# Kernel optimization log

Measured on AMD Instinct MI355X. Metric: run time of the kernel, lower is better.

## Reference

```python
import jax, jax.numpy as jnp
import numpy as np

N = 50000    # nodes
E = 800000   # edges (avg degree 16)
IN = 256     # in_dim
HID = 256    # hidden_dim
OUT = 128    # out_dim


def setup_inputs() -> dict:
    key = jax.random.key(0)
    ks = jax.random.split(key, 9)
    features = jax.random.normal(ks[0], (N, IN), jnp.float32)
    src = jax.random.randint(ks[1], (E,), 0, N, jnp.int32)
    dst = jax.random.randint(ks[2], (E,), 0, N, jnp.int32)
    noise = jax.random.normal(ks[3], (N, OUT), jnp.float32)
    def glorot(k, shape, fan):
        return jax.random.normal(k, shape, jnp.float32) / np.float32(np.sqrt(fan))
    W1 = glorot(ks[4], (IN, HID), IN);  b1 = jnp.zeros((HID,), jnp.float32)
    W2 = glorot(ks[5], (HID, OUT), HID); b2 = jnp.zeros((OUT,), jnp.float32)
    W3 = glorot(ks[6], (HID, OUT), HID); b3 = jnp.zeros((OUT,), jnp.float32)
    fcW = glorot(ks[7], (HID, IN), IN)   # nn.Linear(in_dim, hidden_dim).weight: [HID, IN]
    return dict(features=features, noise=noise, W1=W1, b1=b1, W2=W2, b2=b2,
                W3=W3, b3=b3, fcW=fcW, src=src, dst=dst)


def _gcn(x, W, b, src, dst, out_norm, in_norm):
    """DGL GraphConv norm='both': D_out^{-1/2} A D_in^{-1/2} X W + b."""
    x = x * out_norm[:, None]          # scale src features by out-deg^{-1/2}
    x = x @ W                          # dense transform (order commutes with SpMM)
    agg = jax.ops.segment_sum(x[src], dst, num_segments=N)  # sparse aggregate
    return agg * in_norm[:, None] + b


def reference(features, noise, W1, b1, W2, b2, W3, b3, fcW, src, dst):
    ones = jnp.ones((E,), jnp.float32)
    out_deg = jax.ops.segment_sum(ones, src, num_segments=N)
    in_deg = jax.ops.segment_sum(ones, dst, num_segments=N)
    out_norm = jnp.maximum(out_deg, 1.0) ** -0.5
    in_norm = jnp.maximum(in_deg, 1.0) ** -0.5

    h = jax.nn.relu(_gcn(features, W1, b1, src, dst, out_norm, in_norm))
    mean = jax.nn.relu(_gcn(h, W2, b2, src, dst, out_norm, in_norm))
    log_std = _gcn(h, W3, b3, src, dst, out_norm, in_norm)  # identity activation
    z = mean + noise * jnp.exp(log_std)
    seq_fts = features @ fcW.T
    return z, h, seq_fts
```

## Files before the change

kernel.cpp:

```cpp
#include <hip/hip_runtime.h>
#include <hip/hip_bf16.h>
#include <stdint.h>

#define IN_DIM 256
#define HID_DIM 256
#define OUT_DIM 128

typedef __attribute__((ext_vector_type(8))) short short8;
typedef __attribute__((ext_vector_type(4))) float floatx4;

__device__ __forceinline__ float bf2f(ushort u) {
  union { uint32_t i; float f; } v; v.i = ((uint32_t)u) << 16; return v.f;
}
__device__ __forceinline__ ushort f2bf(float f) {
  union { float f; uint32_t u; } v; v.f = f;
  uint32_t u = v.u;
  uint32_t r = u + 0x7fffu + ((u >> 16) & 1u);
  return (ushort)(r >> 16);
}

__global__ void f2b_kernel(const float* __restrict__ in, ushort* __restrict__ out, int n) {
  int base = (blockIdx.x * 256 + threadIdx.x) * 4;
  if (base < n) {
    float4 v = *(const float4*)(in + base);
    ushort4 o;
    o.x = f2bf(v.x); o.y = f2bf(v.y); o.z = f2bf(v.z); o.w = f2bf(v.w);
    *(ushort4*)(out + base) = o;
  }
}

__global__ void deg_kernel(const int* __restrict__ src, const int* __restrict__ dst,
                           int* __restrict__ out_deg, int* __restrict__ in_deg, int E) {
  int e = blockIdx.x * 256 + threadIdx.x;
  if (e < E) {
    atomicAdd(&out_deg[src[e]], 1);
    atomicAdd(&in_deg[dst[e]], 1);
  }
}

__global__ void norm_kernel(const int* __restrict__ out_deg, const int* __restrict__ in_deg,
                            float* __restrict__ out_norm, float* __restrict__ in_norm, int N) {
  int n = blockIdx.x * 256 + threadIdx.x;
  if (n < N) {
    int od = out_deg[n]; if (od < 1) od = 1;
    int id = in_deg[n];  if (id < 1) id = 1;
    out_norm[n] = rsqrtf((float)od);
    in_norm[n]  = rsqrtf((float)id);
  }
}

__global__ void scan_sums(const int* __restrict__ deg, int* __restrict__ chunk_sum, int n) {
  __shared__ int lds[256];
  int b = blockIdx.x, t = threadIdx.x;
  int base = b * 1024 + t * 4;
  int s = 0;
  if (base + 3 < n) {
    int4 v = *(const int4*)(deg + base);
    s = v.x + v.y + v.z + v.w;
  } else {
    for (int i = 0; i < 4; ++i) if (base + i < n) s += deg[base + i];
  }
  lds[t] = s;
  __syncthreads();
  for (int off = 128; off > 0; off >>= 1) {
    if (t < off) lds[t] += lds[t + off];
    __syncthreads();
  }
  if (t == 0) chunk_sum[b] = lds[0];
}

__global__ void scan_chunks(const int* __restrict__ chunk_sum, int* __restrict__ chunk_off,
                            int nchunks, int* __restrict__ row_ptr) {
  __shared__ int lds[256];
  int t = threadIdx.x;
  int v = (t < nchunks) ? chunk_sum[t] : 0;
  lds[t] = v;
  __syncthreads();
  for (int off = 1; off < 256; off <<= 1) {
    int add = (t >= off) ? lds[t - off] : 0;
    __syncthreads();
    lds[t] += add;
    __syncthreads();
  }
  if (t < nchunks) chunk_off[t] = lds[t] - v;
  if (t == 0) row_ptr[0] = 0;
}

__global__ void scan_final(const int* __restrict__ deg, const int* __restrict__ chunk_off,
                           int* __restrict__ row_ptr, int n) {
  __shared__ int lds[256];
  int b = blockIdx.x, t = threadIdx.x;
  int base = b * 1024 + t * 4;
  int v[4]; int s = 0;
#pragma unroll
  for (int i = 0; i < 4; ++i) { v[i] = (base + i < n) ? deg[base + i] : 0; s += v[i]; }
  lds[t] = s;
  __syncthreads();
  for (int off = 1; off < 256; off <<= 1) {
    int add = (t >= off) ? lds[t - off] : 0;
    __syncthreads();
    lds[t] += add;
    __syncthreads();
  }
  int run = lds[t] - s + chunk_off[b];
#pragma unroll
  for (int i = 0; i < 4; ++i) {
    run += v[i];
    if (base + i < n) row_ptr[base + i + 1] = run;
  }
}

__global__ void fill_kernel(const int* __restrict__ src, const int* __restrict__ dst,
                            const int* __restrict__ row_ptr, int* __restrict__ fill_cnt,
                            const float* __restrict__ out_norm,
                            int* __restrict__ edge_src, float* __restrict__ edge_w, int E) {
  int e = blockIdx.x * 256 + threadIdx.x;
  if (e < E) {
    int d = dst[e];
    int s = src[e];
    int pos = row_ptr[d] + atomicAdd(&fill_cnt[d], 1);
    edge_src[pos] = s;
    edge_w[pos] = out_norm[s];
  }
}

__global__ void prep_weights(const float* __restrict__ W1, const float* __restrict__ W2,
                             const float* __restrict__ W3, const float* __restrict__ b2,
                             const float* __restrict__ b3, const float* __restrict__ fcW,
                             ushort* __restrict__ W1T, ushort* __restrict__ WcT,
                             float* __restrict__ bcat, ushort* __restrict__ fcWb) {
  int k = blockIdx.x;
  int n = threadIdx.x;
  W1T[n * 256 + k] = f2bf(W1[k * 256 + n]);
  WcT[n * 256 + k] = f2bf((n < 128) ? W2[k * 128 + n] : W3[k * 128 + (n - 128)]);
  fcWb[k * 256 + n] = f2bf(fcW[k * 256 + n]);
  if (k == 0) bcat[n] = (n < 128) ? b2[n] : b3[n - 128];
}

__global__ __launch_bounds__(256) void agg_kernel(
    const ushort* __restrict__ x, const int* __restrict__ row_ptr,
    const int* __restrict__ edge_src, const float* __restrict__ edge_w,
    const float* __restrict__ in_norm, ushort* __restrict__ out, int N) {
  int wave = threadIdx.x >> 6, lane = threadIdx.x & 63;
  int n = blockIdx.x * 4 + wave;
  if (n >= N) return;
  int half = lane >> 5;
  int hl = lane & 31;
  int start = row_ptr[n], end = row_ptr[n + 1];
  float acc[8];
#pragma unroll
  for (int k = 0; k < 8; ++k) acc[k] = 0.f;

  for (int base = start; base < end; base += 4) {
    int i0 = base + half;
    int i1 = base + 2 + half;
    int s0 = 0, s1 = 0; float w0 = 0.f, w1 = 0.f;
    if (i0 < end) { s0 = edge_src[i0]; w0 = edge_w[i0]; }
    if (i1 < end) { s1 = edge_src[i1]; w1 = edge_w[i1]; }
    uint4 v0 = *(const uint4*)&x[(size_t)s0 * 256 + hl * 8];
    uint4 v1 = *(const uint4*)&x[(size_t)s1 * 256 + hl * 8];
    const uint32_t* p0 = (const uint32_t*)&v0;
    const uint32_t* p1 = (const uint32_t*)&v1;
#pragma unroll
    for (int k = 0; k < 4; ++k) {
      acc[2 * k]     += bf2f((ushort)(p0[k] & 0xffffu)) * w0;
      acc[2 * k + 1] += bf2f((ushort)(p0[k] >> 16)) * w0;
      acc[2 * k]     += bf2f((ushort)(p1[k] & 0xffffu)) * w1;
      acc[2 * k + 1] += bf2f((ushort)(p1[k] >> 16)) * w1;
    }
  }
#pragma unroll
  for (int k = 0; k < 8; ++k) acc[k] += __shfl_xor(acc[k], 32, 64);

  if (half == 0) {
    float inn = in_norm[n];
    uint4 o;
    uint32_t* po = (uint32_t*)&o;
#pragma unroll
    for (int k = 0; k < 4; ++k) {
      po[k] = ((uint32_t)f2bf(acc[2 * k + 1] * inn) << 16) |
              (uint32_t)f2bf(acc[2 * k] * inn);
    }
    *(uint4*)&out[(size_t)n * 256 + hl * 8] = o;
  }
}

__global__ __launch_bounds__(256) void gemm_kernel(
    const ushort* __restrict__ A, const ushort* __restrict__ BT,
    const float* __restrict__ bias, float* __restrict__ C32,
    ushort* __restrict__ Cbf, int M, int Nout, int relu) {
  __shared__ alignas(16) ushort A_lds[128 * 72];
  __shared__ alignas(16) ushort B_lds[128 * 72];
  int t = threadIdx.x;
  int m0 = blockIdx.x * 128;
  int n0 = blockIdx.y * 128;
  int wave = t >> 6, lane = t & 63;
  int wm = (wave >> 1) * 64, wn = (wave & 1) * 64;
  int l15 = lane & 15, quad = lane >> 4;

  floatx4 acc[4][4];
#pragma unroll
  for (int i = 0; i < 4; ++i)
#pragma unroll
    for (int j = 0; j < 4; ++j) acc[i][j] = (floatx4)(0.f);

  for (int kc = 0; kc < 256; kc += 64) {
#pragma unroll
    for (int r = 0; r < 4; ++r) {
      int idx = t + r * 256;
      int row = idx >> 3;
      int c8 = (idx & 7) << 3;
      int grow = m0 + row; if (grow > M - 1) grow = M - 1;
      uint4 va = *(const uint4*)(A + (size_t)grow * 256 + kc + c8);
      *(uint4*)&A_lds[row * 72 + c8] = va;
      uint4 vb = *(const uint4*)(BT + (size_t)(n0 + row) * 256 + kc + c8);
      *(uint4*)&B_lds[row * 72 + c8] = vb;
    }
    __syncthreads();
#pragma unroll
    for (int ko = 0; ko < 2; ++ko) {
      short8 a[4], b[4];
#pragma unroll
      for (int i = 0; i < 4; ++i) {
        a[i] = *(const short8*)&A_lds[(wm + i * 16 + l15) * 72 + ko * 32 + quad * 8];
        b[i] = *(const short8*)&B_lds[(wn + i * 16 + l15) * 72 + ko * 32 + quad * 8];
      }
#pragma unroll
      for (int i = 0; i < 4; ++i)
#pragma unroll
        for (int j = 0; j < 4; ++j)
          acc[i][j] = __builtin_amdgcn_mfma_f32_16x16x32_bf16(a[i], b[j], acc[i][j], 0, 0, 0);
    }
    __syncthreads();
  }

#pragma unroll
  for (int i = 0; i < 4; ++i) {
#pragma unroll
    for (int j = 0; j < 4; ++j) {
      int col = n0 + wn + j * 16 + l15;
      float bv = bias ? bias[col] : 0.f;
#pragma unroll
      for (int r = 0; r < 4; ++r) {
        int row = m0 + wm + i * 16 + quad * 4 + r;
        if (row < M) {
          float v = acc[i][j][r] + bv;
          if (relu) v = fmaxf(v, 0.f);
          size_t o = (size_t)row * Nout + col;
          if (C32) C32[o] = v;
          if (Cbf) Cbf[o] = f2bf(v);
        }
      }
    }
  }
}

__global__ void z_kernel(const ushort* __restrict__ tmp, const float* __restrict__ noise,
                         float* __restrict__ z, int N) {
  int idx = blockIdx.x * 256 + threadIdx.x;
  if (idx < N * OUT_DIM) {
    int n = idx >> 7, c = idx & 127;
    float m = bf2f(tmp[(size_t)n * 256 + c]);
    float ls = bf2f(tmp[(size_t)n * 256 + 128 + c]);
    float zz = fmaxf(m, 0.f) + noise[idx] * expf(ls);
    z[idx] = zz;
  }
}

extern "C" void kernel_launch(void* const* d_in, const int* in_sizes, int n_in,
                              void* d_out, int out_size, void* d_ws, size_t ws_size,
                              hipStream_t stream) {
  const float* features = (const float*)d_in[0];
  const float* noise    = (const float*)d_in[1];
  const float* W1 = (const float*)d_in[2];
  const float* b1 = (const float*)d_in[3];
  const float* W2 = (const float*)d_in[4];
  const float* b2 = (const float*)d_in[5];
  const float* W3 = (const float*)d_in[6];
  const float* b3 = (const float*)d_in[7];
  const float* fcW = (const float*)d_in[8];
  const int* src = (const int*)d_in[9];
  const int* dst = (const int*)d_in[10];
  const int N = in_sizes[0] / IN_DIM;
  const int E = in_sizes[9];

  float* out = (float*)d_out;
  float* z_out = out;
  float* h_out = out + (size_t)N * OUT_DIM;
  float* s_out = h_out + (size_t)N * HID_DIM;

  char* w = (char*)d_ws;
  auto carve = [&](size_t bytes) {
    char* p = w;
    w += (bytes + 255) & ~(size_t)255;
    return p;
  };
  ushort* feat_bf = (ushort*)carve((size_t)N * 256 * 2);
  ushort* h_bf    = (ushort*)carve((size_t)N * 256 * 2);
  ushort* agg_buf = (ushort*)carve((size_t)N * 256 * 2);
  ushort* tmp_bf  = (ushort*)carve((size_t)N * 256 * 2);
  ushort* W1T  = (ushort*)carve(256 * 256 * 2);
  ushort* WcT  = (ushort*)carve(256 * 256 * 2);
  ushort* fcWb = (ushort*)carve(256 * 256 * 2);
  float*  bcat = (float*)carve(256 * 4);
  int* degs    = (int*)carve((size_t)3 * N * 4);
  int* out_deg = degs;
  int* in_deg  = degs + N;
  int* fill_cnt = degs + 2 * N;
  float* out_norm = (float*)carve((size_t)N * 4);
  float* in_norm  = (float*)carve((size_t)N * 4);
  int* row_ptr  = (int*)carve((size_t)(N + 1) * 4);
  int* edge_src = (int*)carve((size_t)E * 4);
  float* edge_w = (float*)carve((size_t)E * 4);
  int* chunk_sum = (int*)carve(256 * 4);
  int* chunk_off = (int*)carve(256 * 4);

  const int nchunks = (N + 1023) / 1024;

  hipMemsetAsync(degs, 0, (size_t)3 * N * 4, stream);
  deg_kernel<<<(E + 255) / 256, 256, 0, stream>>>(src, dst, out_deg, in_deg, E);
  norm_kernel<<<(N + 255) / 256, 256, 0, stream>>>(out_deg, in_deg, out_norm, in_norm, N);
  scan_sums<<<nchunks, 256, 0, stream>>>(in_deg, chunk_sum, N);
  scan_chunks<<<1, 256, 0, stream>>>(chunk_sum, chunk_off, nchunks, row_ptr);
  scan_final<<<nchunks, 256, 0, stream>>>(in_deg, chunk_off, row_ptr, N);
  fill_kernel<<<(E + 255) / 256, 256, 0, stream>>>(src, dst, row_ptr, fill_cnt, out_norm,
                                                   edge_src, edge_w, E);

  f2b_kernel<<<((N * 256 / 4) + 255) / 256, 256, 0, stream>>>(features, feat_bf, N * 256);
  prep_weights<<<256, 256, 0, stream>>>(W1, W2, W3, b2, b3, fcW, W1T, WcT, bcat, fcWb);

  dim3 ggrid((N + 127) / 128, 2);
  agg_kernel<<<(N + 3) / 4, 256, 0, stream>>>(feat_bf, row_ptr, edge_src, edge_w, in_norm, agg_buf, N);
  gemm_kernel<<<ggrid, 256, 0, stream>>>(agg_buf, W1T, b1, h_out, h_bf, N, 256, 1);
  agg_kernel<<<(N + 3) / 4, 256, 0, stream>>>(h_bf, row_ptr, edge_src, edge_w, in_norm, agg_buf, N);
  gemm_kernel<<<ggrid, 256, 0, stream>>>(agg_buf, WcT, bcat, (float*)nullptr, tmp_bf, N, 256, 0);
  z_kernel<<<(N * OUT_DIM + 255) / 256, 256, 0, stream>>>(tmp_bf, noise, z_out, N);
  gemm_kernel<<<ggrid, 256, 0, stream>>>(feat_bf, fcWb, (const float*)nullptr, s_out, (ushort*)nullptr, N, 256, 0);
}
```

Measured before the change: 587.9 us.

## Fuse z computation into GEMM epilogue, widen GEMM tile, drop norm kernel

The GEMM now computes a full 128x256 output tile per block, so mean and log_std columns sit in the same block, and the reparameterization z = relu(mean) + noise*exp(log_std) is applied in the epilogue. This removes the separate z kernel and the bf16 temporary round trip. The norm kernel is also removed, and degree-to-rsqrt conversion is computed inline in the fill and aggregation kernels. The wider tile uses more LDS and accumulator registers (launch bounds request 2 blocks), which may lower occupancy, and the grid is halved.

New measurement: 547.8 us. 1.07x faster.

```diff
diff --git a/kernel.cpp b/kernel.cpp
--- a/kernel.cpp
+++ b/kernel.cpp
@@ -1,6 +1,7 @@
 #include <hip/hip_runtime.h>
 #include <hip/hip_bf16.h>
 #include <stdint.h>
+#include <math.h>
 
 #define IN_DIM 256
 #define HID_DIM 256
@@ -35,17 +36,6 @@
   if (e < E) {
     atomicAdd(&out_deg[src[e]], 1);
     atomicAdd(&in_deg[dst[e]], 1);
-  }
-}
-
-__global__ void norm_kernel(const int* __restrict__ out_deg, const int* __restrict__ in_deg,
-                            float* __restrict__ out_norm, float* __restrict__ in_norm, int N) {
-  int n = blockIdx.x * 256 + threadIdx.x;
-  if (n < N) {
-    int od = out_deg[n]; if (od < 1) od = 1;
-    int id = in_deg[n];  if (id < 1) id = 1;
-    out_norm[n] = rsqrtf((float)od);
-    in_norm[n]  = rsqrtf((float)id);
   }
 }
 
@@ -112,15 +102,16 @@
 
 __global__ void fill_kernel(const int* __restrict__ src, const int* __restrict__ dst,
                             const int* __restrict__ row_ptr, int* __restrict__ fill_cnt,
-                            const float* __restrict__ out_norm,
+                            const int* __restrict__ out_deg,
                             int* __restrict__ edge_src, float* __restrict__ edge_w, int E) {
   int e = blockIdx.x * 256 + threadIdx.x;
   if (e < E) {
     int d = dst[e];
     int s = src[e];
     int pos = row_ptr[d] + atomicAdd(&fill_cnt[d], 1);
+    int od = out_deg[s]; if (od < 1) od = 1;
     edge_src[pos] = s;
-    edge_w[pos] = out_norm[s];
+    edge_w[pos] = rsqrtf((float)od);
   }
 }
 
@@ -140,7 +131,7 @@
 __global__ __launch_bounds__(256) void agg_kernel(
     const ushort* __restrict__ x, const int* __restrict__ row_ptr,
     const int* __restrict__ edge_src, const float* __restrict__ edge_w,
-    const float* __restrict__ in_norm, ushort* __restrict__ out, int N) {
+    const int* __restrict__ in_deg, ushort* __restrict__ out, int N) {
   int wave = threadIdx.x >> 6, lane = threadIdx.x & 63;
   int n = blockIdx.x * 4 + wave;
   if (n >= N) return;
@@ -173,7 +164,8 @@
   for (int k = 0; k < 8; ++k) acc[k] += __shfl_xor(acc[k], 32, 64);
 
   if (half == 0) {
-    float inn = in_norm[n];
+    int id = in_deg[n]; if (id < 1) id = 1;
+    float inn = rsqrtf((float)id);
     uint4 o;
     uint32_t* po = (uint32_t*)&o;
 #pragma unroll
@@ -185,85 +177,98 @@
   }
 }
 
-__global__ __launch_bounds__(256) void gemm_kernel(
+__global__ __launch_bounds__(256, 2) void gemm_kernel(
     const ushort* __restrict__ A, const ushort* __restrict__ BT,
-    const float* __restrict__ bias, float* __restrict__ C32,
-    ushort* __restrict__ Cbf, int M, int Nout, int relu) {
+    const float* __restrict__ bias, const float* __restrict__ noise,
+    float* __restrict__ C32, ushort* __restrict__ Cbf, int M, int mode) {
   __shared__ alignas(16) ushort A_lds[128 * 72];
-  __shared__ alignas(16) ushort B_lds[128 * 72];
+  __shared__ alignas(16) ushort B_lds[256 * 72];
   int t = threadIdx.x;
   int m0 = blockIdx.x * 128;
-  int n0 = blockIdx.y * 128;
   int wave = t >> 6, lane = t & 63;
-  int wm = (wave >> 1) * 64, wn = (wave & 1) * 64;
+  int wm = wave * 32;
   int l15 = lane & 15, quad = lane >> 4;
 
-  floatx4 acc[4][4];
-#pragma unroll
-  for (int i = 0; i < 4; ++i)
-#pragma unroll
-    for (int j = 0; j < 4; ++j) acc[i][j] = (floatx4)(0.f);
+  floatx4 acc[2][16];
+#pragma unroll
+  for (int i = 0; i < 2; ++i)
+#pragma unroll
+    for (int j = 0; j < 16; ++j) acc[i][j] = (floatx4)(0.f);
 
   for (int kc = 0; kc < 256; kc += 64) {
 #pragma unroll
     for (int r = 0; r < 4; ++r) {
       int idx = t + r * 256;
       int row = idx >> 3;
-      int c8 = (idx & 7) << 3;
+      int c = (idx & 7) << 3;
       int grow = m0 + row; if (grow > M - 1) grow = M - 1;
-      uint4 va = *(const uint4*)(A + (size_t)grow * 256 + kc + c8);
-      *(uint4*)&A_lds[row * 72 + c8] = va;
-      uint4 vb = *(const uint4*)(BT + (size_t)(n0 + row) * 256 + kc + c8);
-      *(uint4*)&B_lds[row * 72 + c8] = vb;
+      *(uint4*)&A_lds[row * 72 + c] = *(const uint4*)(A + (size_t)grow * 256 + kc + c);
+    }
+#pragma unroll
+    for (int r = 0; r < 8; ++r) {
+      int idx = t + r * 256;
+      int row = idx >> 3;
+      int c = (idx & 7) << 3;
+      *(uint4*)&B_lds[row * 72 + c] = *(const uint4*)(BT + (size_t)row * 256 + kc + c);
     }
     __syncthreads();
 #pragma unroll
     for (int ko = 0; ko < 2; ++ko) {
-      short8 a[4], b[4];
-#pragma unroll
-      for (int i = 0; i < 4; ++i) {
+      short8 a[2];
+#pragma unroll
+      for (int i = 0; i < 2; ++i)
         a[i] = *(const short8*)&A_lds[(wm + i * 16 + l15) * 72 + ko * 32 + quad * 8];
-        b[i] = *(const short8*)&B_lds[(wn + i * 16 + l15) * 72 + ko * 32 + quad * 8];
+#pragma unroll
+      for (int j = 0; j < 16; ++j) {
+        short8 b = *(const short8*)&B_lds[(j * 16 + l15) * 72 + ko * 32 + quad * 8];
+#pragma unroll
+        for (int i = 0; i < 2; ++i)
+          acc[i][j] = __builtin_amdgcn_mfma_f32_16x16x32_bf16(a[i], b, acc[i][j], 0, 0, 0);
       }
-#pragma unroll
-      for (int i = 0; i < 4; ++i)
-#pragma unroll
-        for (int j = 0; j < 4; ++j)
-          acc[i][j] = __builtin_amdgcn_mfma_f32_16x16x32_bf16(a[i], b[j], acc[i][j], 0, 0, 0);
-    }
-    __syncthreads();
-  }
-
-#pragma unroll
-  for (int i = 0; i < 4; ++i) {
-#pragma unroll
-    for (int j = 0; j < 4; ++j) {
-      int col = n0 + wn + j * 16 + l15;
-      float bv = bias ? bias[col] : 0.f;
-#pragma unroll
-      for (int r = 0; r < 4; ++r) {
-        int row = m0 + wm + i * 16 + quad * 4 + r;
-        if (row < M) {
-          float v = acc[i][j][r] + bv;
-          if (relu) v = fmaxf(v, 0.f);
-          size_t o = (size_t)row * Nout + col;
-          if (C32) C32[o] = v;
-          if (Cbf) Cbf[o] = f2bf(v);
+    }
+    __syncthreads();
+  }
+
+  if (mode == 1) {
+#pragma unroll
+    for (int i = 0; i < 2; ++i) {
+#pragma unroll
+      for (int j = 0; j < 8; ++j) {
+        int col = j * 16 + l15;
+        float bm = bias[col];
+        float bl = bias[col + 128];
+#pragma unroll
+        for (int r = 0; r < 4; ++r) {
+          int row = m0 + wm + i * 16 + quad * 4 + r;
+          if (row < M) {
+            float mean = acc[i][j][r] + bm;
+            float ls = acc[i][j + 8][r] + bl;
+            size_t o = (size_t)row * 128 + col;
+            C32[o] = fmaxf(mean, 0.f) + noise[o] * expf(ls);
+          }
         }
       }
     }
-  }
-}
-
-__global__ void z_kernel(const ushort* __restrict__ tmp, const float* __restrict__ noise,
-                         float* __restrict__ z, int N) {
-  int idx = blockIdx.x * 256 + threadIdx.x;
-  if (idx < N * OUT_DIM) {
-    int n = idx >> 7, c = idx & 127;
-    float m = bf2f(tmp[(size_t)n * 256 + c]);
-    float ls = bf2f(tmp[(size_t)n * 256 + 128 + c]);
-    float zz = fmaxf(m, 0.f) + noise[idx] * expf(ls);
-    z[idx] = zz;
+  } else {
+#pragma unroll
+    for (int i = 0; i < 2; ++i) {
+#pragma unroll
+      for (int j = 0; j < 16; ++j) {
+        int col = j * 16 + l15;
+        float bv = (mode == 0) ? bias[col] : 0.f;
+#pragma unroll
+        for (int r = 0; r < 4; ++r) {
+          int row = m0 + wm + i * 16 + quad * 4 + r;
+          if (row < M) {
+            float v = acc[i][j][r] + bv;
+            if (mode == 0) v = fmaxf(v, 0.f);
+            size_t o = (size_t)row * 256 + col;
+            C32[o] = v;
+            if (mode == 0) Cbf[o] = f2bf(v);
+          }
+        }
+      }
+    }
   }
 }
 
@@ -298,7 +303,6 @@
   ushort* feat_bf = (ushort*)carve((size_t)N * 256 * 2);
   ushort* h_bf    = (ushort*)carve((size_t)N * 256 * 2);
   ushort* agg_buf = (ushort*)carve((size_t)N * 256 * 2);
-  ushort* tmp_bf  = (ushort*)carve((size_t)N * 256 * 2);
   ushort* W1T  = (ushort*)carve(256 * 256 * 2);
   ushort* WcT  = (ushort*)carve(256 * 256 * 2);
   ushort* fcWb = (ushort*)carve(256 * 256 * 2);
@@ -307,8 +311,6 @@
   int* out_deg = degs;
   int* in_deg  = degs + N;
   int* fill_cnt = degs + 2 * N;
-  float* out_norm = (float*)carve((size_t)N * 4);
-  float* in_norm  = (float*)carve((size_t)N * 4);
   int* row_ptr  = (int*)carve((size_t)(N + 1) * 4);
   int* edge_src = (int*)carve((size_t)E * 4);
   float* edge_w = (float*)carve((size_t)E * 4);
@@ -319,21 +321,22 @@
 
   hipMemsetAsync(degs, 0, (size_t)3 * N * 4, stream);
   deg_kernel<<<(E + 255) / 256, 256, 0, stream>>>(src, dst, out_deg, in_deg, E);
-  norm_kernel<<<(N + 255) / 256, 256, 0, stream>>>(out_deg, in_deg, out_norm, in_norm, N);
   scan_sums<<<nchunks, 256, 0, stream>>>(in_deg, chunk_sum, N);
   scan_chunks<<<1, 256, 0, stream>>>(chunk_sum, chunk_off, nchunks, row_ptr);
   scan_final<<<nchunks, 256, 0, stream>>>(in_deg, chunk_off, row_ptr, N);
-  fill_kernel<<<(E + 255) / 256, 256, 0, stream>>>(src, dst, row_ptr, fill_cnt, out_norm,
+  fill_kernel<<<(E + 255) / 256, 256, 0, stream>>>(src, dst, row_ptr, fill_cnt, out_deg,
                                                    edge_src, edge_w, E);
 
   f2b_kernel<<<((N * 256 / 4) + 255) / 256, 256, 0, stream>>>(features, feat_bf, N * 256);
   prep_weights<<<256, 256, 0, stream>>>(W1, W2, W3, b2, b3, fcW, W1T, WcT, bcat, fcWb);
 
-  dim3 ggrid((N + 127) / 128, 2);
-  agg_kernel<<<(N + 3) / 4, 256, 0, stream>>>(feat_bf, row_ptr, edge_src, edge_w, in_norm, agg_buf, N);
-  gemm_kernel<<<ggrid, 256, 0, stream>>>(agg_buf, W1T, b1, h_out, h_bf, N, 256, 1);
-  agg_kernel<<<(N + 3) / 4, 256, 0, stream>>>(h_bf, row_ptr, edge_src, edge_w, in_norm, agg_buf, N);
-  gemm_kernel<<<ggrid, 256, 0, stream>>>(agg_buf, WcT, bcat, (float*)nullptr, tmp_bf, N, 256, 0);
-  z_kernel<<<(N * OUT_DIM + 255) / 256, 256, 0, stream>>>(tmp_bf, noise, z_out, N);
-  gemm_kernel<<<ggrid, 256, 0, stream>>>(feat_bf, fcWb, (const float*)nullptr, s_out, (ushort*)nullptr, N, 256, 0);
-}
+  int gblocks = (N + 127) / 128;
+  agg_kernel<<<(N + 3) / 4, 256, 0, stream>>>(feat_bf, row_ptr, edge_src, edge_w, in_deg, agg_buf, N);
+  gemm_kernel<<<gblocks, 256, 0, stream>>>(agg_buf, W1T, b1, (const float*)nullptr,
+                                           h_out, h_bf, N, 0);
+  agg_kernel<<<(N + 3) / 4, 256, 0, stream>>>(h_bf, row_ptr, edge_src, edge_w, in_deg, agg_buf, N);
+  gemm_kernel<<<gblocks, 256, 0, stream>>>(agg_buf, WcT, bcat, noise,
+                                           z_out, (ushort*)nullptr, N, 1);
+  gemm_kernel<<<gblocks, 256, 0, stream>>>(feat_bf, fcWb, (const float*)nullptr,
+                                           (const float*)nullptr, s_out, (ushort*)nullptr, N, 2);
+}
```
